# Optimization experiments

Hardware: AMD Instinct MI355X
Metric: run time of the kernel (lower is better)

Reference implementation:

```python
import jax, jax.numpy as jnp
import numpy as np

P = 10      # qubits
LQ = 4      # re-uploading layers
B = 4096    # batch
HID = 32    # readout hidden
DIM = 2 ** P


def _rz(t):
    t = jnp.asarray(t, jnp.float32)
    e = jnp.exp(-0.5j * t.astype(jnp.complex64))
    z = jnp.zeros_like(e)
    return jnp.stack([jnp.stack([e, z], -1), jnp.stack([z, jnp.conj(e)], -1)], -2)


def _rx(t):
    t = jnp.asarray(t, jnp.float32)
    c = jnp.cos(0.5 * t).astype(jnp.complex64)
    s = jnp.sin(0.5 * t).astype(jnp.complex64)
    return jnp.stack([jnp.stack([c, -1j * s], -1), jnp.stack([-1j * s, c], -1)], -2)


def _ry(t):
    t = jnp.asarray(t, jnp.float32)
    c = jnp.cos(0.5 * t).astype(jnp.complex64)
    s = jnp.sin(0.5 * t).astype(jnp.complex64)
    return jnp.stack([jnp.stack([c, -s], -1), jnp.stack([s, c], -1)], -2)


def _apply_1q(state, U, k):
    # state [B, 2^P] complex, U [B,2,2]; wire 0 = most-significant bit (PennyLane order)
    b = state.shape[0]
    s = state.reshape(b, 2 ** k, 2, -1)
    s = jnp.einsum('bij,bajc->baic', U, s)
    return s.reshape(b, -1)


def _apply_cnot(state, c, t):
    b = state.shape[0]
    a, d = min(c, t), max(c, t)
    s = state.reshape(b, 2 ** a, 2, 2 ** (d - a - 1), 2, -1)
    if c == a:  # control = smaller wire index (axis 2), target at axis 4
        hi = jnp.flip(s[:, :, 1], axis=3)  # [b,pre,mid,2,post] -> flip target bit
        s = jnp.stack([s[:, :, 0], hi], axis=2)
    else:       # control = larger wire index (axis 4), target at axis 2
        hi = jnp.flip(s[:, :, :, :, 1], axis=2)  # [b,pre,2,mid,post] -> flip target bit
        s = jnp.stack([s[:, :, :, :, 0], hi], axis=4)
    return s.reshape(b, -1)


def _meas_signs(p):
    # rows 0..p-1: Z_k signs; rows p..2p-1: Z_k Z_{(k+1)%p} signs
    idx = np.arange(2 ** p)
    bits = (idx[None, :] >> (p - 1 - np.arange(p)[:, None])) & 1
    z = (1.0 - 2.0 * bits).astype(np.float32)            # [p, 2^p]
    zz = z * np.roll(z, -1, axis=0)                      # [p, 2^p]
    return jnp.asarray(np.concatenate([z, zz], axis=0))  # [2p, 2^p]


MEAS = _meas_signs(P)


def _circuit_feats(theta, rot_weights, enc_scale, enc_bias):
    b = theta.shape[0]
    # Hadamard on every wire of |0...0> -> uniform superposition
    state = jnp.full((b, DIM), 1.0 / np.sqrt(DIM), dtype=jnp.complex64)
    for l in range(LQ):
        for k in range(P):
            t0 = enc_scale[l, k, 0] * theta[:, k] + enc_bias[l, k, 0]
            t1 = enc_scale[l, k, 1] * theta[:, k] + enc_bias[l, k, 1]
            U_enc = jnp.einsum('bij,bjk->bik', _rx(t1), _rz(t0))  # RX(t1) RZ(t0)
            w = rot_weights[l, k]
            # PennyLane Rot(phi,theta,omega) = RZ(omega) RY(theta) RZ(phi)
            U_rot = _rz(w[2]) @ _ry(w[1]) @ _rz(w[0])
            U = jnp.einsum('ij,bjk->bik', U_rot, U_enc)
            state = _apply_1q(state, U, k)
        for k in range(P):
            state = _apply_cnot(state, k, (k + 1) % P)
    probs = jnp.abs(state) ** 2              # [B, 2^P]
    return probs @ MEAS.T                    # [B, 2P] expectation values


def setup_inputs() -> dict:
    key = jax.random.key(0)
    ks = jax.random.split(key, 4)
    theta = jax.random.uniform(ks[0], (B, P), jnp.float32, -np.pi, np.pi)
    rot_weights = 0.02 * jax.random.normal(ks[1], (LQ, P, 3), dtype=jnp.float32)
    enc_scale = jnp.ones((LQ, P, 2), jnp.float32)   # clamp(0.5,1.5) of ones = ones
    enc_bias = jnp.zeros((LQ, P, 2), jnp.float32)
    n_meas = 2 * P
    W1 = jax.random.normal(ks[2], (HID, n_meas), dtype=jnp.float32) / np.sqrt(n_meas)
    b1 = jnp.zeros((HID,), jnp.float32)
    W2 = jax.random.normal(ks[3], (1, HID), dtype=jnp.float32) / np.sqrt(HID)
    b2 = jnp.zeros((1,), jnp.float32)
    return dict(theta=theta, rot_weights=rot_weights, enc_scale=enc_scale,
                enc_bias=enc_bias, W1=W1, b1=b1, W2=W2, b2=b2)


def reference(theta, rot_weights, enc_scale, enc_bias, W1, b1, W2, b2):
    feats = _circuit_feats(theta, rot_weights, enc_scale, enc_bias)
    h = jax.nn.silu(feats @ W1.T + b1)
    return (h @ W2.T + b2)[:, 0]  # [B]
```

## Files before the change

kernel.cpp:

```cpp
#include <hip/hip_runtime.h>
#include <math.h>

#define NQ   10
#define NLAY 4
#define BATCH 4096
#define HID  32
#define NM   20

typedef float    f2  __attribute__((ext_vector_type(2)));
typedef unsigned u2v __attribute__((ext_vector_type(2)));

struct Tables {
    unsigned col[NLAY + 1][NQ];
    unsigned row[NLAY + 1][NQ];
};

constexpr Tables make_tables() {
    Tables t{};
    unsigned col[NQ] = {}, row[NQ] = {};
    for (int k = 0; k < NQ; ++k) { col[k] = 1u << (NQ - 1 - k); row[k] = 1u << (NQ - 1 - k); }
    for (int l = 0; l <= NLAY; ++l) {
        for (int k = 0; k < NQ; ++k) { t.col[l][k] = col[k]; t.row[l][k] = row[k]; }
        for (int k = 0; k < NQ; ++k) {
            int c = k, tg = (k + 1) % NQ;
            col[c] ^= col[tg];
            row[tg] ^= row[c];
        }
    }
    return t;
}

static constexpr Tables TB = make_tables();

struct cpx { float x, y; };
__device__ __forceinline__ cpx cxmul(cpx a, cpx b) {
    return { fmaf(a.x, b.x, -a.y * b.y), fmaf(a.x, b.y, a.y * b.x) };
}

__device__ __forceinline__ f2 mk2(float a, float b) { f2 r; r[0] = a; r[1] = b; return r; }
__device__ __forceinline__ f2 ffma(f2 a, f2 b, f2 c) { return __builtin_elementwise_fma(a, b, c); }

__device__ __forceinline__ f2 cmac(f2 acc, f2 a, f2 b) {
    acc = ffma(mk2(a[0], a[0]), b, acc);
    acc = ffma(mk2(-a[1], a[1]), mk2(b[1], b[0]), acc);
    return acc;
}

template<int CTRL>
__device__ __forceinline__ float dppf(float x) {
    return __int_as_float(__builtin_amdgcn_update_dpp(
        0, __float_as_int(x), CTRL, 0xF, 0xF, true));
}

template<unsigned M>
__device__ __forceinline__ float dpplo(float x) {
    static_assert(M < 16u, "dpplo handles masks 0..15");
    if constexpr (M == 0u)       return x;
    else if constexpr (M == 1u)  return dppf<0xB1>(x);
    else if constexpr (M == 2u)  return dppf<0x4E>(x);
    else if constexpr (M == 3u)  return dppf<0x1B>(x);
    else if constexpr (M == 7u)  return dppf<0x141>(x);
    else if constexpr (M == 8u)  return dppf<0x128>(x);
    else if constexpr (M == 15u) return dppf<0x140>(x);
    else if constexpr (M == 4u)  return dppf<0x141>(dppf<0x1B>(x));
    else if constexpr (M == 5u)  return dppf<0x141>(dppf<0x4E>(x));
    else if constexpr (M == 6u)  return dppf<0x141>(dppf<0xB1>(x));
    else if constexpr (M == 9u)  return dppf<0x128>(dppf<0xB1>(x));
    else if constexpr (M == 10u) return dppf<0x128>(dppf<0x4E>(x));
    else if constexpr (M == 11u) return dppf<0x128>(dppf<0x1B>(x));
    else if constexpr (M == 12u) return dppf<0x140>(dppf<0x1B>(x));
    else if constexpr (M == 13u) return dppf<0x140>(dppf<0x4E>(x));
    else                         return dppf<0x140>(dppf<0xB1>(x));
}

__device__ __forceinline__ float redfold16(float x) {
#if __has_builtin(__builtin_amdgcn_permlane16_swap)
    u2v r = __builtin_amdgcn_permlane16_swap(__float_as_uint(x), __float_as_uint(x), false, false);
    return __uint_as_float(r[0]) + __uint_as_float(r[1]);
#else
    return x + __shfl_xor(x, 16);
#endif
}

template<unsigned M>
__device__ __forceinline__ float xlane(float x) {
    if constexpr (M == 0u) return x;
    else if constexpr ((M & 16u) != 0u)
        return __int_as_float(__builtin_amdgcn_ds_swizzle(
            __float_as_int(x), (int)((M << 10) | 0x1F)));
    else return dpplo<M>(x);
}

template<int L, int K>
__device__ __forceinline__ void apply_gate(f2 (&st)[32], const float4 (*gm)[2],
                                           const int lane) {
    constexpr unsigned v     = TB.col[L][K];
    constexpr unsigned m     = TB.row[L][K];
    constexpr unsigned vlane = (v >> 5) & 31u;
    constexpr int      vr    = (int)(v & 31u);
    constexpr unsigned mlane = (m >> 5) & 31u;
    constexpr int      mr    = (int)(m & 31u);
    constexpr int      gi    = L * NQ + K;

    int laneP = 0;
    if constexpr (mlane != 0u) laneP = __popc((unsigned)lane & mlane) & 1;
    const float4 A = gm[gi][laneP];
    const f2 ocA = mk2(A.x, A.y), pcA = mk2(A.z, A.w);
    f2 ocB = ocA, pcB = pcA;
    if constexpr (mr != 0) {
        const float4 B = gm[gi][laneP ^ 1];
        ocB = mk2(B.x, B.y); pcB = mk2(B.z, B.w);
    }

    #pragma unroll
    for (int r = 0; r < 32; ++r) {
        const int r2 = r ^ vr;
        if (r2 < r) continue;
        f2 p_r, p_r2;
        if constexpr (vlane != 0u) {
            p_r = mk2(xlane<vlane>(st[r2][0]), xlane<vlane>(st[r2][1]));
            if (r2 != r)
                p_r2 = mk2(xlane<vlane>(st[r][0]), xlane<vlane>(st[r][1]));
        } else {
            p_r = st[r2];
            p_r2 = st[r];
        }
        {
            const int pr = __builtin_popcount((unsigned)(r & mr)) & 1;
            const f2 oc = pr ? ocB : ocA;
            const f2 pc = pr ? pcB : pcA;
            f2 acc = mk2(0.f, 0.f);
            acc = cmac(acc, oc, st[r]);
            acc = cmac(acc, pc, p_r);
            if (r2 != r) {
                const int pr2 = __builtin_popcount((unsigned)(r2 & mr)) & 1;
                const f2 oc2 = pr2 ? ocB : ocA;
                const f2 pc2 = pr2 ? pcB : pcA;
                f2 acc2 = mk2(0.f, 0.f);
                acc2 = cmac(acc2, oc2, st[r2]);
                acc2 = cmac(acc2, pc2, p_r2);
                st[r2] = acc2;
            }
            st[r] = acc;
        }
    }
}

__global__ __launch_bounds__(256, 2)
void qrh_kernel(
    const float* __restrict__ theta, const float* __restrict__ rotw,
    const float* __restrict__ escale, const float* __restrict__ ebias,
    const float* __restrict__ W1, const float* __restrict__ b1,
    const float* __restrict__ W2, const float* __restrict__ b2,
    float* __restrict__ out)
{
    __shared__ float4 gmat[8 * NLAY * NQ][2];
    __shared__ float4 wtab[8][NQ];

    const int tid  = threadIdx.x;
    const int lane = tid & 63;
    const int wv   = tid >> 6;
    const int e    = (wv << 1) | (lane >> 5);
    const int b    = blockIdx.x * 8 + e;

    for (int g = tid; g < 8 * NLAY * NQ; g += 256) {
        const int ge = g / (NLAY * NQ);
        const int gg = g % (NLAY * NQ);
        const int l = gg / NQ, k = gg % NQ;
        const int gb = blockIdx.x * 8 + ge;
        const float th = theta[gb * NQ + k];
        const int e2 = (l * NQ + k) * 2;
        const float t0 = escale[e2 + 0] * th + ebias[e2 + 0];
        const float t1 = escale[e2 + 1] * th + ebias[e2 + 1];
        float sn0, c0, sn1, c1;
        __sincosf(0.5f * t0, &sn0, &c0);
        __sincosf(0.5f * t1, &sn1, &c1);
        const f2 E00 = mk2( c1 * c0,  -c1 * sn0);
        const f2 E01 = mk2( sn1 * sn0, -sn1 * c0);
        const f2 E10 = mk2(-sn1 * sn0, -sn1 * c0);
        const f2 E11 = mk2( c1 * c0,   c1 * sn0);
        const int r3 = (l * NQ + k) * 3;
        const float w0 = rotw[r3 + 0], w1 = rotw[r3 + 1], w2 = rotw[r3 + 2];
        float cw, sw, ca0, sa0, ca1, sa1;
        __sincosf(0.5f * w1, &sw, &cw);
        __sincosf(0.5f * (w0 + w2), &sa0, &ca0);
        __sincosf(0.5f * (w0 - w2), &sa1, &ca1);
        const f2 R00 = mk2( cw * ca0, -cw * sa0);
        const f2 R01 = mk2(-sw * ca1, -sw * sa1);
        const f2 R10 = mk2( sw * ca1, -sw * sa1);
        const f2 R11 = mk2( cw * ca0,  cw * sa0);
        auto cm = [](f2 a, f2 bb) { return mk2(a[0]*bb[0] - a[1]*bb[1], a[0]*bb[1] + a[1]*bb[0]); };
        const f2 U00 = cm(R00, E00) + cm(R01, E10);
        const f2 U01 = cm(R00, E01) + cm(R01, E11);
        const f2 U10 = cm(R10, E00) + cm(R11, E10);
        const f2 U11 = cm(R10, E01) + cm(R11, E11);
        gmat[g][0] = make_float4(U00[0], U00[1], U01[0], U01[1]);
        gmat[g][1] = make_float4(U11[0], U11[1], U10[0], U10[1]);
        if (l == 0) {
            const float inv = 0.70710678118654752f;
            const f2 al = (U00 + U01) * inv;
            const f2 be = (U10 + U11) * inv;
            wtab[ge][k] = make_float4(al[0], al[1], be[0], be[1]);
        }
    }
    __syncthreads();

    if (wv & 1) { __builtin_amdgcn_s_sleep(10); __builtin_amdgcn_s_sleep(10); }

    const int hl = lane & 31;
    f2 st[32];
    {
        cpx pre;
        {
            const float4 q = wtab[e][0];
            pre = ((hl >> 4) & 1) ? cpx{q.z, q.w} : cpx{q.x, q.y};
            #pragma unroll
            for (int k = 1; k < 5; ++k) {
                const float4 t = wtab[e][k];
                const cpx w_ = ((hl >> (4 - k)) & 1) ? cpx{t.z, t.w} : cpx{t.x, t.y};
                pre = cxmul(pre, w_);
            }
        }
        const float4 q5 = wtab[e][5], q6 = wtab[e][6], q7 = wtab[e][7];
        const float4 q8 = wtab[e][8], q9 = wtab[e][9];
        const cpx w5[2] = {{q5.x, q5.y}, {q5.z, q5.w}};
        const cpx w6[2] = {{q6.x, q6.y}, {q6.z, q6.w}};
        const cpx w7[2] = {{q7.x, q7.y}, {q7.z, q7.w}};
        const cpx w8[2] = {{q8.x, q8.y}, {q8.z, q8.w}};
        const cpx w9[2] = {{q9.x, q9.y}, {q9.z, q9.w}};
        cpx a7[8];
        #pragma unroll
        for (int j = 0; j < 8; ++j)
            a7[j] = cxmul(cxmul(cxmul(pre, w5[j >> 2]), w6[(j >> 1) & 1]), w7[j & 1]);
        #pragma unroll
        for (int r = 0; r < 32; ++r) {
            const cpx t = cxmul(cxmul(a7[r >> 2], w8[(r >> 1) & 1]), w9[r & 1]);
            st[r] = mk2(t.x, t.y);
        }
    }

    const float4 (*gm)[2] = &gmat[e * NLAY * NQ];

    #define GATE(L,K) apply_gate<L,K>(st, gm, lane);
    #define LAYER(L) GATE(L,0) GATE(L,1) GATE(L,2) GATE(L,3) GATE(L,4) \
                     GATE(L,5) GATE(L,6) GATE(L,7) GATE(L,8) GATE(L,9)
    LAYER(1)
    LAYER(2)
    LAYER(3)
    #undef LAYER
    #undef GATE

    float w[32];
    #pragma unroll
    for (int r = 0; r < 32; ++r) {
        const f2 sq = st[r] * st[r];
        w[r] = sq[0] + sq[1];
    }
    #pragma unroll
    for (int bit = 1; bit < 32; bit <<= 1) {
        #pragma unroll
        for (int j = 0; j < 32; ++j) {
            if (!(j & bit)) {
                const float a = w[j], c = w[j | bit];
                w[j] = a + c; w[j | bit] = a - c;
            }
        }
    }

    float feats[NM];
    #pragma unroll
    for (int f = 0; f < NM; ++f) {
        const unsigned M = (f < NQ) ? TB.row[NLAY][f]
                                    : (TB.row[NLAY][f - NQ] ^ TB.row[NLAY][(f - NQ + 1) % NQ]);
        const unsigned Mlane = (M >> 5) & 31u;
        const int Mr = (int)(M & 31u);
        const float s = w[Mr];
        const int lsgn = __popc((unsigned)lane & Mlane) & 1;
        feats[f] = lsgn ? -s : s;
    }
    #pragma unroll
    for (int f = 0; f < NM; ++f) {
        float v = feats[f];
        v += dppf<0xB1>(v);
        v += dppf<0x4E>(v);
        v += dppf<0x141>(v);
        v += dppf<0x128>(v);
        v = redfold16(v);
        feats[f] = v;
    }

    float part;
    {
        float acc = b1[hl];
        #pragma unroll
        for (int mm = 0; mm < NM; ++mm) acc = fmaf(feats[mm], W1[hl * NM + mm], acc);
        const float sg = 1.f / (1.f + __expf(-acc));
        part = acc * sg * W2[hl];
    }
    part += dppf<0xB1>(part);
    part += dppf<0x4E>(part);
    part += dppf<0x141>(part);
    part += dppf<0x128>(part);
    part = redfold16(part);
    if (hl == 0) out[b] = part + b2[0];
}

extern "C" void kernel_launch(void* const* d_in, const int* in_sizes, int n_in,
                              void* d_out, int out_size, void* d_ws, size_t ws_size,
                              hipStream_t stream) {
    (void)in_sizes; (void)n_in; (void)out_size; (void)d_ws; (void)ws_size;
    const float* theta = (const float*)d_in[0];
    const float* rotw  = (const float*)d_in[1];
    const float* esc   = (const float*)d_in[2];
    const float* ebi   = (const float*)d_in[3];
    const float* W1    = (const float*)d_in[4];
    const float* b1    = (const float*)d_in[5];
    const float* W2    = (const float*)d_in[6];
    const float* b2    = (const float*)d_in[7];
    float* out = (float*)d_out;

    qrh_kernel<<<BATCH / 8, 256, 0, stream>>>(theta, rotw, esc, ebi, W1, b1, W2, b2, out);
}
```

Baseline: 92.11 us.

## Remap state index basis so cross-lane gates use full-vector shuffle path

Applies a linear change of basis to the amplitude-index tables, a prefix-XOR transform for columns and an adjacent-XOR transform for rows, so that each gate's partner pattern maps differently onto registers and lanes. Adds a separate gate path for masks touching lane bit 16 that shuffles all 32 partner amplitudes up front, then does a straight per-register update instead of pairwise handling. Rebuilds the initial product state to match the new basis. This aims to cut the number and cost of cross-lane exchanges, at the cost of higher register pressure from the extra 32-entry partner array.

Result: slower. 95.09 us (+3.2%).

```diff
diff --git a/kernel.cpp b/kernel.cpp
--- a/kernel.cpp
+++ b/kernel.cpp
@@ -14,6 +14,24 @@
     unsigned col[NLAY + 1][NQ];
     unsigned row[NLAY + 1][NQ];
 };
+
+constexpr unsigned tr_col(unsigned v) {
+    unsigned s = 0, pref = 0;
+    for (int j = 0; j < 9; ++j) { pref ^= (v >> (9 - j)) & 1u; s |= pref << j; }
+    unsigned tot = pref ^ (v & 1u);
+    s |= tot << 9;
+    return s;
+}
+constexpr unsigned tr_row(unsigned m) {
+    unsigned s = 0;
+    for (int j = 0; j < 9; ++j) {
+        unsigned a = (m >> (9 - j)) & 1u;
+        unsigned b = (m >> (8 - j)) & 1u;
+        s |= (a ^ b) << j;
+    }
+    s |= (m & 1u) << 9;
+    return s;
+}
 
 constexpr Tables make_tables() {
     Tables t{};
@@ -27,6 +45,11 @@
             row[tg] ^= row[c];
         }
     }
+    for (int l = 0; l <= NLAY; ++l)
+        for (int k = 0; k < NQ; ++k) {
+            t.col[l][k] = tr_col(t.col[l][k]);
+            t.row[l][k] = tr_row(t.row[l][k]);
+        }
     return t;
 }
 
@@ -112,36 +135,55 @@
         ocB = mk2(B.x, B.y); pcB = mk2(B.z, B.w);
     }
 
-    #pragma unroll
-    for (int r = 0; r < 32; ++r) {
-        const int r2 = r ^ vr;
-        if (r2 < r) continue;
-        f2 p_r, p_r2;
-        if constexpr (vlane != 0u) {
-            p_r = mk2(xlane<vlane>(st[r2][0]), xlane<vlane>(st[r2][1]));
-            if (r2 != r)
-                p_r2 = mk2(xlane<vlane>(st[r][0]), xlane<vlane>(st[r][1]));
-        } else {
-            p_r = st[r2];
-            p_r2 = st[r];
-        }
-        {
+    if constexpr ((vlane & 16u) != 0u) {
+        f2 pv[32];
+        #pragma unroll
+        for (int r = 0; r < 32; ++r) {
+            const f2 q = st[r ^ vr];
+            pv[r] = mk2(xlane<vlane>(q[0]), xlane<vlane>(q[1]));
+        }
+        #pragma unroll
+        for (int r = 0; r < 32; ++r) {
             const int pr = __builtin_popcount((unsigned)(r & mr)) & 1;
             const f2 oc = pr ? ocB : ocA;
             const f2 pc = pr ? pcB : pcA;
             f2 acc = mk2(0.f, 0.f);
             acc = cmac(acc, oc, st[r]);
-            acc = cmac(acc, pc, p_r);
-            if (r2 != r) {
-                const int pr2 = __builtin_popcount((unsigned)(r2 & mr)) & 1;
-                const f2 oc2 = pr2 ? ocB : ocA;
-                const f2 pc2 = pr2 ? pcB : pcA;
-                f2 acc2 = mk2(0.f, 0.f);
-                acc2 = cmac(acc2, oc2, st[r2]);
-                acc2 = cmac(acc2, pc2, p_r2);
-                st[r2] = acc2;
+            acc = cmac(acc, pc, pv[r]);
+            st[r] = acc;
+        }
+    } else {
+        #pragma unroll
+        for (int r = 0; r < 32; ++r) {
+            const int r2 = r ^ vr;
+            if (r2 < r) continue;
+            f2 p_r, p_r2;
+            if constexpr (vlane != 0u) {
+                p_r = mk2(xlane<vlane>(st[r2][0]), xlane<vlane>(st[r2][1]));
+                if (r2 != r)
+                    p_r2 = mk2(xlane<vlane>(st[r][0]), xlane<vlane>(st[r][1]));
+            } else {
+                p_r = st[r2];
+                p_r2 = st[r];
             }
-            st[r] = acc;
+            {
+                const int pr = __builtin_popcount((unsigned)(r & mr)) & 1;
+                const f2 oc = pr ? ocB : ocA;
+                const f2 pc = pr ? pcB : pcA;
+                f2 acc = mk2(0.f, 0.f);
+                acc = cmac(acc, oc, st[r]);
+                acc = cmac(acc, pc, p_r);
+                if (r2 != r) {
+                    const int pr2 = __builtin_popcount((unsigned)(r2 & mr)) & 1;
+                    const f2 oc2 = pr2 ? ocB : ocA;
+                    const f2 pc2 = pr2 ? pcB : pcA;
+                    f2 acc2 = mk2(0.f, 0.f);
+                    acc2 = cmac(acc2, oc2, st[r2]);
+                    acc2 = cmac(acc2, pc2, p_r2);
+                    st[r2] = acc2;
+                }
+                st[r] = acc;
+            }
         }
     }
 }
@@ -210,31 +252,29 @@
     const int hl = lane & 31;
     f2 st[32];
     {
-        cpx pre;
-        {
-            const float4 q = wtab[e][0];
-            pre = ((hl >> 4) & 1) ? cpx{q.z, q.w} : cpx{q.x, q.y};
-            #pragma unroll
-            for (int k = 1; k < 5; ++k) {
-                const float4 t = wtab[e][k];
-                const cpx w_ = ((hl >> (4 - k)) & 1) ? cpx{t.z, t.w} : cpx{t.x, t.y};
-                pre = cxmul(pre, w_);
-            }
-        }
-        const float4 q5 = wtab[e][5], q6 = wtab[e][6], q7 = wtab[e][7];
-        const float4 q8 = wtab[e][8], q9 = wtab[e][9];
-        const cpx w5[2] = {{q5.x, q5.y}, {q5.z, q5.w}};
-        const cpx w6[2] = {{q6.x, q6.y}, {q6.z, q6.w}};
-        const cpx w7[2] = {{q7.x, q7.y}, {q7.z, q7.w}};
-        const cpx w8[2] = {{q8.x, q8.y}, {q8.z, q8.w}};
-        const cpx w9[2] = {{q9.x, q9.y}, {q9.z, q9.w}};
-        cpx a7[8];
-        #pragma unroll
-        for (int j = 0; j < 8; ++j)
-            a7[j] = cxmul(cxmul(cxmul(pre, w5[j >> 2]), w6[(j >> 1) & 1]), w7[j & 1]);
+        cpx w_[10][2];
+        #pragma unroll
+        for (int k = 0; k < NQ; ++k) {
+            const float4 q = wtab[e][k];
+            w_[k][0] = {q.x, q.y};
+            w_[k][1] = {q.z, q.w};
+        }
+        const int h0 = hl & 1, h1 = (hl >> 1) & 1, h2 = (hl >> 2) & 1,
+                  h3 = (hl >> 3) & 1, h4 = (hl >> 4) & 1;
+        const cpx PL = cxmul(cxmul(w_[6][h0 ^ h1], w_[7][h1 ^ h2]),
+                             cxmul(w_[8][h2 ^ h3], w_[9][h3 ^ h4]));
+        const cpx PL5[2] = { cxmul(PL, w_[5][h0]), cxmul(PL, w_[5][1 ^ h0]) };
+        cpx G012[8], G34[8];
+        #pragma unroll
+        for (int q = 0; q < 8; ++q) {
+            const int a0 = q & 1, a1 = (q >> 1) & 1, a2 = (q >> 2) & 1;
+            G012[q] = cxmul(cxmul(w_[0][a0], w_[1][a0 ^ a1]), w_[2][a1 ^ a2]);
+            G34[q]  = cxmul(w_[3][a0 ^ a1], w_[4][a1 ^ a2]);
+        }
         #pragma unroll
         for (int r = 0; r < 32; ++r) {
-            const cpx t = cxmul(cxmul(a7[r >> 2], w8[(r >> 1) & 1]), w9[r & 1]);
+            const cpx g = cxmul(G012[r & 7], G34[(r >> 2) & 7]);
+            const cpx t = cxmul(PL5[(r >> 4) & 1], g);
             st[r] = mk2(t.x, t.y);
         }
     }
```
